# Kernel tuning notes

Hardware: AMD Instinct MI355X
Metric: run time of the kernel (lower is better)

The kernel has to match this reference:

```python
import jax, jax.numpy as jnp
import numpy as np

S, B_BOX, N_CLASS = 7, 2, 20
L_COORD, L_NOOBJ = 5.0, 0.5
BATCH = 4096
C = 5 * B_BOX + N_CLASS  # 30


def setup_inputs() -> dict:
    key = jax.random.key(0)
    k1, k2, k3, k4 = jax.random.split(key, 4)
    # coords/w/h/classes strictly positive (sqrt is applied to raw values)
    y = jax.random.uniform(k1, (BATCH, S, S, C), minval=0.05, maxval=0.95, dtype=jnp.float32)
    # confidence channels must be exactly 0/1 (mask tests == 1)
    conf0 = jax.random.bernoulli(k3, 0.3, (BATCH, S, S)).astype(jnp.float32)
    conf1 = jax.random.bernoulli(k4, 0.3, (BATCH, S, S)).astype(jnp.float32)
    y = y.at[..., 0].set(conf0).at[..., 5].set(conf1)
    y_h = jax.random.uniform(k2, (BATCH, S, S, C), minval=0.05, maxval=0.95, dtype=jnp.float32)
    return {"y": y, "y_h": y_h}


def _loss(y, y_h):
    b_sz = y.shape[0]
    conf_idx = np.arange(B_BOX) * 5  # [0, 5]
    y_conf = y[..., conf_idx]        # [B,S,S,b]
    yh_conf = y_h[..., conf_idx]
    mf = (y_conf == 1.0).astype(y.dtype)  # obj mask per box, constant wrt grads
    dconf = (y_conf - yh_conf) ** 2
    loss_obj = jnp.sum(dconf * mf)
    loss_noobj = jnp.sum(dconf * (1.0 - mf))

    loss_coord = jnp.zeros((), y.dtype)
    loss_prob = jnp.zeros((), y.dtype)
    for k in range(B_BOX):  # static small loop over boxes
        mk = mf[..., k]  # [B,S,S]
        base = 5 * k
        dxy = (y[..., base + 1] - y_h[..., base + 1]) ** 2 \
            + (y[..., base + 2] - y_h[..., base + 2]) ** 2
        dwh = (jnp.sqrt(y[..., base + 3]) - jnp.sqrt(y_h[..., base + 3])) ** 2 \
            + (jnp.sqrt(y[..., base + 4]) - jnp.sqrt(y_h[..., base + 4])) ** 2
        loss_coord = loss_coord + jnp.sum((dxy + dwh) * mk)

        # prob term: slice from k*5+5 to end (faithful to original, for k=0 this
        # includes box-2's 5 entries), softmax over the masked batch dimension.
        tail = y[..., base + 5:]
        tail_h = y_h[..., base + 5:]
        mkb = mk[..., None]  # [B,S,S,1]
        neg = jnp.where(mkb > 0, tail_h, -jnp.inf)
        m = jnp.max(neg, axis=0)                       # [S,S,Ct]
        m_safe = jnp.where(jnp.isfinite(m), m, 0.0)    # guard empty columns
        p = jnp.exp(tail_h - m_safe) * mkb
        denom = jnp.sum(p, axis=0)
        sm = p / jnp.where(denom > 0, denom, 1.0)
        loss_prob = loss_prob + jnp.sum((tail - sm) ** 2 * mkb)

    loss = loss_obj + L_NOOBJ * loss_noobj + L_COORD * loss_coord + loss_prob
    return loss / b_sz


def reference(y, y_h):
    return _loss(y, y_h)
```

## Files before the change

kernel.cpp:

```cpp
#include <hip/hip_runtime.h>
#include <math.h>

#define CC 30
#define NBATCH 4096
#define NIJ 49
#define NPAIR 1225
#define PSTR 7352
#define F4TOT (PSTR / 4)
#define THREADS 512
#define SLABF4 1470


__global__ __launch_bounds__(THREADS)
void yolo_main(const float* __restrict__ y, const float* __restrict__ yh,
               float* __restrict__ scal, float* __restrict__ parts, int nwg)
{
    __shared__ __align__(16) float tY[4 * 1470];
    __shared__ __align__(16) float tH[4 * 1470];
    __shared__ float scr[4][8];

    const int tid = threadIdx.x;
    const int wg  = blockIdx.x;
    const int bpw = NBATCH / nwg;
    const int nslab = bpw >> 2;

    const int i0 = tid, i1 = tid + 512;
    const int i2r = tid + 1024;
    const int i2  = (i2r < SLABF4) ? i2r : (SLABF4 - 1);
    const bool w2 = (i2r < SLABF4);

    int  ijv[3], cv[3], pr[3];
    bool val[3];
    #pragma unroll
    for (int i = 0; i < 3; i++) {
        int p = tid + i * THREADS;
        val[i] = (p < NPAIR);
        pr[i]  = p;
        int pp = val[i] ? p : 0;
        ijv[i] = pp / 25;
        cv[i]  = 5 + pp % 25;
    }

    float D0[3] = {0,0,0}, B0[3] = {0,0,0}, C0[3] = {0,0,0};
    float D1[3] = {0,0,0}, B1[3] = {0,0,0}, C1[3] = {0,0,0};
    float obj = 0.f, noobj = 0.f, coord = 0.f, tt = 0.f;

    const float4* Yg = (const float4*)y;
    const float4* Hg = (const float4*)yh;
    float4* tY4 = (float4*)tY;
    float4* tH4 = (float4*)tH;

    {
        const size_t f4 = (size_t)((wg * bpw) >> 2) * SLABF4;
        float4 a0 = Yg[f4+i0], a1 = Yg[f4+i1], a2 = Yg[f4+i2];
        float4 b0 = Hg[f4+i0], b1 = Hg[f4+i1], b2 = Hg[f4+i2];
        tY4[i0] = a0; tY4[i1] = a1; if (w2) tY4[i2] = a2;
        tH4[i0] = b0; tH4[i1] = b1; if (w2) tH4[i2] = b2;
    }
    __syncthreads();

    float4 ry0, ry1, ry2, rh0, rh1, rh2;

    for (int s = 0; s < nslab; s++) {
        if (s + 1 < nslab) {
            const size_t nf4 = (size_t)((wg * bpw + (s+1)*4) >> 2) * SLABF4;
            ry0 = Yg[nf4+i0]; ry1 = Yg[nf4+i1]; ry2 = Yg[nf4+i2];
            rh0 = Hg[nf4+i0]; rh1 = Hg[nf4+i1]; rh2 = Hg[nf4+i2];
        }

        if (tid < 4 * NIJ) {
            const int base = tid * CC;
            float y0 = tY[base],     h0 = tH[base];
            float y5 = tY[base + 5], h5 = tH[base + 5];
            float d0 = y0 - h0; d0 *= d0;
            float d5 = y5 - h5; d5 *= d5;
            const bool m0 = (y0 == 1.0f), m1 = (y5 == 1.0f);
            obj   += (m0 ? d0 : 0.f) + (m1 ? d5 : 0.f);
            noobj += (m0 ? 0.f : d0) + (m1 ? 0.f : d5);
            if (m0) {
                float a  = tY[base + 1] - tH[base + 1];
                float b2 = tY[base + 2] - tH[base + 2];
                float c1 = sqrtf(tY[base + 3]) - sqrtf(tH[base + 3]);
                float c2 = sqrtf(tY[base + 4]) - sqrtf(tH[base + 4]);
                coord += a * a + b2 * b2 + c1 * c1 + c2 * c2;
            }
            if (m1) {
                float a  = tY[base + 6] - tH[base + 6];
                float b2 = tY[base + 7] - tH[base + 7];
                float c1 = sqrtf(tY[base + 8]) - sqrtf(tH[base + 8]);
                float c2 = sqrtf(tY[base + 9]) - sqrtf(tH[base + 9]);
                coord += a * a + b2 * b2 + c1 * c1 + c2 * c2;
            }
        }

        #pragma unroll
        for (int b = 0; b < 4; b++) {
            #pragma unroll
            for (int i = 0; i < 3; i++) {
                if (!val[i]) continue;
                const int cb = b * 1470 + ijv[i] * CC;
                const float w0 = (tY[cb] == 1.0f) ? 1.f : 0.f;
                const float wk = (cv[i] >= 10 && tY[cb + 5] == 1.0f) ? 1.f : 0.f;
                const float t  = tY[cb + cv[i]];
                const float th = tH[cb + cv[i]];
                const float e  = __expf(th);
                const float te = t * e, ee = e * e, t2 = t * t;
                D0[i] = fmaf(e,  w0, D0[i]);
                B0[i] = fmaf(te, w0, B0[i]);
                C0[i] = fmaf(ee, w0, C0[i]);
                D1[i] = fmaf(e,  wk, D1[i]);
                B1[i] = fmaf(te, wk, B1[i]);
                C1[i] = fmaf(ee, wk, C1[i]);
                tt = fmaf(t2, w0 + wk, tt);
            }
        }
        __syncthreads();
        if (s + 1 < nslab) {
            tY4[i0] = ry0; tY4[i1] = ry1; if (w2) tY4[i2] = ry2;
            tH4[i0] = rh0; tH4[i1] = rh1; if (w2) tH4[i2] = rh2;
        }
        __syncthreads();
    }

    float* pp = parts + (size_t)wg * PSTR;
    #pragma unroll
    for (int i = 0; i < 3; i++) {
        if (!val[i]) continue;
        const int p = pr[i];
        pp[p]            = D0[i];
        pp[NPAIR + p]    = B0[i];
        pp[2*NPAIR + p]  = C0[i];
        pp[3*NPAIR + p]  = D1[i];
        pp[4*NPAIR + p]  = B1[i];
        pp[5*NPAIR + p]  = C1[i];
    }

    const int lane = tid & 63, wv = tid >> 6;
    #pragma unroll
    for (int off = 32; off > 0; off >>= 1) {
        obj   += __shfl_down(obj,   off);
        noobj += __shfl_down(noobj, off);
        coord += __shfl_down(coord, off);
        tt    += __shfl_down(tt,    off);
    }
    if (lane == 0) { scr[0][wv] = obj; scr[1][wv] = noobj; scr[2][wv] = coord; scr[3][wv] = tt; }
    __syncthreads();
    if (tid < 4) {
        float sacc = 0.f;
        #pragma unroll
        for (int w = 0; w < THREADS / 64; w++) sacc += scr[tid][w];
        scal[wg * 4 + tid] = sacc;
    }
}

__global__ __launch_bounds__(512)
void yolo_reduce(const float* __restrict__ parts, float* __restrict__ parts2, int nwg)
{
    const int lane = threadIdx.x & 63;
    const int sub  = threadIdx.x >> 6;
    const int f4i  = blockIdx.x * 64 + lane;
    const int cy   = blockIdx.y;
    const int wpc  = nwg >> 3;
    const int wps  = wpc >> 3;

    float4 s = make_float4(0.f, 0.f, 0.f, 0.f);
    if (f4i < F4TOT) {
        const float* q = parts + (size_t)(cy * wpc + sub * wps) * PSTR + f4i * 4;
        for (int w = 0; w < wps; ++w) {
            float4 a = *(const float4*)q;
            s.x += a.x; s.y += a.y; s.z += a.z; s.w += a.w;
            q += PSTR;
        }
    }
    __shared__ float4 sred[8][64];
    sred[sub][lane] = s;
    __syncthreads();
    if (threadIdx.x < 64 && f4i < F4TOT) {
        float4 t = sred[0][lane];
        #pragma unroll
        for (int c = 1; c < 8; c++) {
            float4 a = sred[c][lane];
            t.x += a.x; t.y += a.y; t.z += a.z; t.w += a.w;
        }
        *(float4*)(parts2 + (size_t)cy * PSTR + f4i * 4) = t;
    }
}

__global__ __launch_bounds__(1024)
void yolo_final(const float* __restrict__ parts2, const float* __restrict__ scal,
                float* __restrict__ out, int nwg)
{
    float v = 0.f;

    for (int s = threadIdx.x; s < NPAIR; s += 1024) {
        const int cidx = s % 25;
        float D0 = 0, B0 = 0, C0 = 0, D1 = 0, B1 = 0, C1 = 0;
        #pragma unroll
        for (int c = 0; c < 8; c++) {
            const float* t = parts2 + (size_t)c * PSTR;
            D0 += t[s];           B0 += t[NPAIR + s];   C0 += t[2*NPAIR + s];
            D1 += t[3*NPAIR + s]; B1 += t[4*NPAIR + s]; C1 += t[5*NPAIR + s];
        }
        if (D0 > 0.f) v += C0 / (D0 * D0) - 2.f * B0 / D0;
        if (cidx >= 5 && D1 > 0.f) v += C1 / (D1 * D1) - 2.f * B1 / D1;
    }

    const float4* s4 = (const float4*)scal;
    for (int w = threadIdx.x; w < nwg; w += 1024) {
        float4 a = s4[w];
        v += a.x + 0.5f * a.y + 5.0f * a.z + a.w;
    }

    __shared__ float sred[16];
    #pragma unroll
    for (int off = 32; off > 0; off >>= 1) v += __shfl_down(v, off);
    const int lane = threadIdx.x & 63, wv = threadIdx.x >> 6;
    if (lane == 0) sred[wv] = v;
    __syncthreads();
    if (threadIdx.x == 0) {
        float tot = 0.f;
        #pragma unroll
        for (int w = 0; w < 16; w++) tot += sred[w];
        out[0] = tot / (float)NBATCH;
    }
}

extern "C" void kernel_launch(void* const* d_in, const int* in_sizes, int n_in,
                              void* d_out, int out_size, void* d_ws, size_t ws_size,
                              hipStream_t stream)
{
    const float* y  = (const float*)d_in[0];
    const float* yh = (const float*)d_in[1];
    float* out    = (float*)d_out;
    float* scal   = (float*)d_ws;
    float* parts2 = (float*)((char*)d_ws + 8192);
    float* parts  = (float*)((char*)d_ws + 243456);

    const size_t per_wg = (size_t)PSTR * sizeof(float);
    int nwg;
    if      (ws_size >= 243456 + 512 * per_wg) nwg = 512;
    else if (ws_size >= 243456 + 256 * per_wg) nwg = 256;
    else                                       nwg = 128;

    yolo_main<<<nwg, THREADS, 0, stream>>>(y, yh, scal, parts, nwg);
    dim3 g2((F4TOT + 63) / 64, 8);
    yolo_reduce<<<g2, 512, 0, stream>>>(parts, parts2, nwg);
    yolo_final<<<1, 1024, 0, stream>>>(parts2, scal, out, nwg);
}
```

Baseline: 29.13 us.

## Double-buffer LDS slabs to drop one barrier per iteration and halve grid size

The shared-memory staging for y and y_h is split into two ping-pong buffers, so the next slab can be written into the idle buffer without waiting on a barrier first. This removes one __syncthreads per slab iteration. The preferred workgroup count also drops from 512 to 256, giving each block more slabs and shrinking the partial-sum buffer the reduce kernel must read. In exchange, LDS use doubles to about 94 KB per block, which limits occupancy, and fewer blocks may underfill the GPU's compute units.

```diff
diff --git a/kernel.cpp b/kernel.cpp
--- a/kernel.cpp
+++ b/kernel.cpp
@@ -9,14 +9,15 @@
 #define F4TOT (PSTR / 4)
 #define THREADS 512
 #define SLABF4 1470
+#define SLABF  5880
 
 
 __global__ __launch_bounds__(THREADS)
 void yolo_main(const float* __restrict__ y, const float* __restrict__ yh,
                float* __restrict__ scal, float* __restrict__ parts, int nwg)
 {
-    __shared__ __align__(16) float tY[4 * 1470];
-    __shared__ __align__(16) float tH[4 * 1470];
+    __shared__ __align__(16) float tY[2][SLABF];
+    __shared__ __align__(16) float tH[2][SLABF];
     __shared__ float scr[4][8];
 
     const int tid = threadIdx.x;
@@ -47,22 +48,24 @@
 
     const float4* Yg = (const float4*)y;
     const float4* Hg = (const float4*)yh;
-    float4* tY4 = (float4*)tY;
-    float4* tH4 = (float4*)tH;
 
     {
         const size_t f4 = (size_t)((wg * bpw) >> 2) * SLABF4;
         float4 a0 = Yg[f4+i0], a1 = Yg[f4+i1], a2 = Yg[f4+i2];
         float4 b0 = Hg[f4+i0], b1 = Hg[f4+i1], b2 = Hg[f4+i2];
-        tY4[i0] = a0; tY4[i1] = a1; if (w2) tY4[i2] = a2;
-        tH4[i0] = b0; tH4[i1] = b1; if (w2) tH4[i2] = b2;
-    }
-    __syncthreads();
-
-    float4 ry0, ry1, ry2, rh0, rh1, rh2;
+        float4* dY = (float4*)tY[0];
+        float4* dH = (float4*)tH[0];
+        dY[i0] = a0; dY[i1] = a1; if (w2) dY[i2] = a2;
+        dH[i0] = b0; dH[i1] = b1; if (w2) dH[i2] = b2;
+    }
+    __syncthreads();
 
     for (int s = 0; s < nslab; s++) {
-        if (s + 1 < nslab) {
+        const float* cy = tY[s & 1];
+        const float* ch = tH[s & 1];
+        const bool pf = (s + 1 < nslab);
+        float4 ry0, ry1, ry2, rh0, rh1, rh2;
+        if (pf) {
             const size_t nf4 = (size_t)((wg * bpw + (s+1)*4) >> 2) * SLABF4;
             ry0 = Yg[nf4+i0]; ry1 = Yg[nf4+i1]; ry2 = Yg[nf4+i2];
             rh0 = Hg[nf4+i0]; rh1 = Hg[nf4+i1]; rh2 = Hg[nf4+i2];
@@ -70,25 +73,25 @@
 
         if (tid < 4 * NIJ) {
             const int base = tid * CC;
-            float y0 = tY[base],     h0 = tH[base];
-            float y5 = tY[base + 5], h5 = tH[base + 5];
+            float y0 = cy[base],     h0 = ch[base];
+            float y5 = cy[base + 5], h5 = ch[base + 5];
             float d0 = y0 - h0; d0 *= d0;
             float d5 = y5 - h5; d5 *= d5;
             const bool m0 = (y0 == 1.0f), m1 = (y5 == 1.0f);
             obj   += (m0 ? d0 : 0.f) + (m1 ? d5 : 0.f);
             noobj += (m0 ? 0.f : d0) + (m1 ? 0.f : d5);
             if (m0) {
-                float a  = tY[base + 1] - tH[base + 1];
-                float b2 = tY[base + 2] - tH[base + 2];
-                float c1 = sqrtf(tY[base + 3]) - sqrtf(tH[base + 3]);
-                float c2 = sqrtf(tY[base + 4]) - sqrtf(tH[base + 4]);
+                float a  = cy[base + 1] - ch[base + 1];
+                float b2 = cy[base + 2] - ch[base + 2];
+                float c1 = sqrtf(cy[base + 3]) - sqrtf(ch[base + 3]);
+                float c2 = sqrtf(cy[base + 4]) - sqrtf(ch[base + 4]);
                 coord += a * a + b2 * b2 + c1 * c1 + c2 * c2;
             }
             if (m1) {
-                float a  = tY[base + 6] - tH[base + 6];
-                float b2 = tY[base + 7] - tH[base + 7];
-                float c1 = sqrtf(tY[base + 8]) - sqrtf(tH[base + 8]);
-                float c2 = sqrtf(tY[base + 9]) - sqrtf(tH[base + 9]);
+                float a  = cy[base + 6] - ch[base + 6];
+                float b2 = cy[base + 7] - ch[base + 7];
+                float c1 = sqrtf(cy[base + 8]) - sqrtf(ch[base + 8]);
+                float c2 = sqrtf(cy[base + 9]) - sqrtf(ch[base + 9]);
                 coord += a * a + b2 * b2 + c1 * c1 + c2 * c2;
             }
         }
@@ -99,10 +102,10 @@
             for (int i = 0; i < 3; i++) {
                 if (!val[i]) continue;
                 const int cb = b * 1470 + ijv[i] * CC;
-                const float w0 = (tY[cb] == 1.0f) ? 1.f : 0.f;
-                const float wk = (cv[i] >= 10 && tY[cb + 5] == 1.0f) ? 1.f : 0.f;
-                const float t  = tY[cb + cv[i]];
-                const float th = tH[cb + cv[i]];
+                const float w0 = (cy[cb] == 1.0f) ? 1.f : 0.f;
+                const float wk = (cv[i] >= 10 && cy[cb + 5] == 1.0f) ? 1.f : 0.f;
+                const float t  = cy[cb + cv[i]];
+                const float th = ch[cb + cv[i]];
                 const float e  = __expf(th);
                 const float te = t * e, ee = e * e, t2 = t * t;
                 D0[i] = fmaf(e,  w0, D0[i]);
@@ -114,10 +117,12 @@
                 tt = fmaf(t2, w0 + wk, tt);
             }
         }
-        __syncthreads();
-        if (s + 1 < nslab) {
-            tY4[i0] = ry0; tY4[i1] = ry1; if (w2) tY4[i2] = ry2;
-            tH4[i0] = rh0; tH4[i1] = rh1; if (w2) tH4[i2] = rh2;
+
+        if (pf) {
+            float4* dY = (float4*)tY[(s + 1) & 1];
+            float4* dH = (float4*)tH[(s + 1) & 1];
+            dY[i0] = ry0; dY[i1] = ry1; if (w2) dY[i2] = ry2;
+            dH[i0] = rh0; dH[i1] = rh1; if (w2) dH[i2] = rh2;
         }
         __syncthreads();
     }
@@ -238,9 +243,9 @@
 
     const size_t per_wg = (size_t)PSTR * sizeof(float);
     int nwg;
-    if      (ws_size >= 243456 + 512 * per_wg) nwg = 512;
-    else if (ws_size >= 243456 + 256 * per_wg) nwg = 256;
-    else                                       nwg = 128;
+    if      (ws_size >= 243456 + 256 * per_wg) nwg = 256;
+    else if (ws_size >= 243456 + 128 * per_wg) nwg = 128;
+    else                                       nwg = 64;
 
     yolo_main<<<nwg, THREADS, 0, stream>>>(y, yh, scal, parts, nwg);
     dim3 g2((F4TOT + 63) / 64, 8);
```

After: 27.48 us (median of 2 runs). 1.06x faster.
